# Kernel tuning notes

Hardware: AMD Instinct MI355X
Metric: run time of the kernel (lower is better)

Reference implementation:

```python
import jax, jax.numpy as jnp
import numpy as np

N_CLASSES = 5  # number of label classes in gts (mode is taken over these)


def setup_inputs() -> dict:
    key = jax.random.key(0)
    k1, k2, k3 = jax.random.split(key, 3)
    B, C, H, W = 4, 128, 512, 512
    n_tokens = 800      # superpixels per image (same for every image)
    max_length = 1024   # fixed sequence length -> pad = 224 per image
    features = jax.random.normal(k1, (B, C, H, W), dtype=jnp.float32)
    gts = jax.random.randint(k2, (B, H, W), 0, N_CLASSES, dtype=jnp.int32)
    segments = jax.random.randint(k3, (B, H, W), 0, n_tokens, dtype=jnp.int32)
    return {"features": features, "gts": gts, "segments": segments,
            "n_tokens": n_tokens, "max_length": max_length}


def reference(features, gts, segments, n_tokens, max_length):
    # Faithful vectorized form of IRGS_Trans.Extract_tokens with
    # mix_images=False, random_tokens=False:
    #   for each superpixel: token = mean of features over its pixels,
    #   label = mode of gts over its pixels; pack per-image into
    #   max_length sequences with zero padding; pads = max_length - n_tokens.
    B, C, H, W = features.shape
    num_seg = B * n_tokens

    # global segment ids (equivalent to the `segments[i] += s + 1` offsetting)
    seg = (segments + jnp.arange(B, dtype=segments.dtype)[:, None, None] * n_tokens).reshape(-1)

    # per-superpixel mean of features: [B*H*W, C] gathered into [B*n_tokens, C]
    feats = jnp.transpose(features, (0, 2, 3, 1)).reshape(-1, C)
    sums = jax.ops.segment_sum(feats, seg, num_segments=num_seg)
    cnt = jax.ops.segment_sum(jnp.ones((seg.shape[0],), feats.dtype), seg,
                              num_segments=num_seg)
    means = sums / jnp.maximum(cnt, 1.0)[:, None]

    # per-superpixel mode of gts via class histogram + argmax
    # (argmax returns the first/smallest class on ties, matching torch.mode)
    onehot = jax.nn.one_hot(gts.reshape(-1), N_CLASSES, dtype=jnp.float32)
    hist = jax.ops.segment_sum(onehot, seg, num_segments=num_seg)
    modes = jnp.argmax(hist, axis=-1).astype(jnp.float32)

    pad = max_length - n_tokens
    tokens = jnp.pad(means.reshape(B, n_tokens, C), ((0, 0), (0, pad), (0, 0)))
    super_labels = jnp.pad(modes.reshape(B, n_tokens), ((0, 0), (0, pad)))
    pads = jnp.full((B, 1), float(pad), dtype=jnp.float32)
    return tokens, super_labels, pads
```

## Files before the change

### kernel.cpp

```cpp
#include <hip/hip_runtime.h>

#define B_    4
#define C_    128
#define H_    512
#define W_    512
#define HW    (H_*W_)
#define NTOK  800
#define MAXLEN 1024
#define NCLS  5
#define NSEG  (B_*NTOK)

#define SCALE      262144.0f
#define INV_SCALE  (1.0f/262144.0f)

#define CG     8
#define NGRP   (C_/CG)
#define CHUNKS 32
#define CHUNK  (HW/CHUNKS)

#define HCHUNKS 64
#define HCHUNK  (HW/HCHUNKS)

#define HBINS   (NTOK*NCLS)
#define SEGBINS (CG*NTOK)

template <bool PARTIAL>
__global__ __launch_bounds__(256) void hist_kernel(const int* __restrict__ seg,
                                                   const int* __restrict__ gts,
                                                   int* __restrict__ hist) {
    __shared__ __align__(16) int lh[HBINS];
    for (int i = threadIdx.x; i < HBINS; i += 256) lh[i] = 0;
    __syncthreads();

    const int chunk = blockIdx.x, b = blockIdx.y;
    const int base = b * HW + chunk * HCHUNK;
    for (int tile = 0; tile < HCHUNK; tile += 1024) {
        const int idx = base + tile + threadIdx.x * 4;
        const int4 s4 = *(const int4*)(seg + idx);
        const int4 g4 = *(const int4*)(gts + idx);
        atomicAdd(&lh[s4.x * NCLS + g4.x], 1);
        atomicAdd(&lh[s4.y * NCLS + g4.y], 1);
        atomicAdd(&lh[s4.z * NCLS + g4.z], 1);
        atomicAdd(&lh[s4.w * NCLS + g4.w], 1);
    }
    __syncthreads();

    if (PARTIAL) {
        int* dst = hist + (size_t)(b * HCHUNKS + chunk) * HBINS;
        for (int i = threadIdx.x; i < HBINS / 4; i += 256)
            ((int4*)dst)[i] = ((const int4*)lh)[i];
    } else {
        int* gh = hist + b * HBINS;
        for (int i = threadIdx.x; i < HBINS; i += 256)
            atomicAdd(&gh[i], lh[i]);
    }
}

template <int NCH>
__global__ __launch_bounds__(256) void finalize_meta_kernel(const int* __restrict__ hist,
                                                            float* __restrict__ invs,
                                                            float* __restrict__ out) {
    const int tid = blockIdx.x * 256 + threadIdx.x;
    const int b = tid >> 10, t = tid & (MAXLEN - 1);
    float label = 0.0f;
    if (t < NTOK) {
        int h[NCLS] = {0, 0, 0, 0, 0};
        const int* hp = hist + (size_t)b * NCH * HBINS + t * NCLS;
#pragma unroll 4
        for (int ch = 0; ch < NCH; ++ch) {
#pragma unroll
            for (int k = 0; k < NCLS; ++k) h[k] += hp[(size_t)ch * HBINS + k];
        }
        int cnt = 0, best = -1, mode = 0;
#pragma unroll
        for (int k = 0; k < NCLS; ++k) {
            cnt += h[k];
            if (h[k] > best) { best = h[k]; mode = k; }
        }
        label = (float)mode;
        invs[b * NTOK + t] = INV_SCALE / (float)max(cnt, 1);
    }
    out[(size_t)B_ * MAXLEN * C_ + tid] = label;
    if (tid < B_) out[(size_t)B_ * MAXLEN * C_ + (size_t)B_ * MAXLEN + tid] =
        (float)(MAXLEN - NTOK);
}

template <bool PARTIAL>
__global__ __launch_bounds__(256, 6) void seg_sum_kernel(const float* __restrict__ feat,
                                                         const int* __restrict__ seg,
                                                         int* __restrict__ sums) {
    __shared__ __align__(16) int lsum[SEGBINS];
    for (int i = threadIdx.x; i < SEGBINS; i += 256) lsum[i] = 0;
    __syncthreads();

    const int chunk = blockIdx.x, grp = blockIdx.y, b = blockIdx.z;
    const int*   segp = seg  + (size_t)b * HW + chunk * CHUNK;
    const float* fp   = feat + ((size_t)b * C_ + (size_t)grp * CG) * HW + chunk * CHUNK;

    for (int tile = 0; tile < CHUNK; tile += 1024) {
        const int idx = tile + threadIdx.x * 4;
        const int4 s4 = *(const int4*)(segp + idx);
        float4 f[CG];
#pragma unroll
        for (int c = 0; c < CG; ++c)
            f[c] = *(const float4*)(fp + (size_t)c * HW + idx);
#pragma unroll
        for (int c = 0; c < CG; ++c) {
            atomicAdd(&lsum[c * NTOK + s4.x], __float2int_rn(f[c].x * SCALE));
            atomicAdd(&lsum[c * NTOK + s4.y], __float2int_rn(f[c].y * SCALE));
            atomicAdd(&lsum[c * NTOK + s4.z], __float2int_rn(f[c].z * SCALE));
            atomicAdd(&lsum[c * NTOK + s4.w], __float2int_rn(f[c].w * SCALE));
        }
    }
    __syncthreads();

    if (PARTIAL) {
        int* dst = sums + (size_t)((b * NGRP + grp) * CHUNKS + chunk) * SEGBINS;
        for (int i = threadIdx.x; i < SEGBINS / 4; i += 256)
            ((int4*)dst)[i] = ((const int4*)lsum)[i];
    } else {
        for (int i = threadIdx.x; i < SEGBINS; i += 256) {
            const int c = i / NTOK, s = i - c * NTOK;
            atomicAdd(&sums[((size_t)(b * NTOK + s)) * C_ + grp * CG + c], lsum[i]);
        }
    }
}

__global__ __launch_bounds__(1024) void reduce_sums_kernel(const int* __restrict__ part,
                                                           int* __restrict__ sums) {
    const int grp = blockIdx.x, b = blockIdx.y;
    const int* p = part + (size_t)(b * NGRP + grp) * CHUNKS * SEGBINS;
    for (int i = threadIdx.x; i < SEGBINS; i += 1024) {
        int acc = 0;
#pragma unroll 8
        for (int ch = 0; ch < CHUNKS; ++ch) acc += p[(size_t)ch * SEGBINS + i];
        const int c = i / NTOK, s = i - c * NTOK;
        sums[((size_t)(b * NTOK + s)) * C_ + grp * CG + c] = acc;
    }
}

__global__ __launch_bounds__(256) void tokens_kernel(const int* __restrict__ sums,
                                                     const float* __restrict__ invs,
                                                     float4* __restrict__ out4) {
    const int i = blockIdx.x * 256 + threadIdx.x;
    const int q = i & 31;
    const int tl = i >> 5;
    const int b = tl >> 10, t = tl & (MAXLEN - 1);
    float4 v = make_float4(0.f, 0.f, 0.f, 0.f);
    if (t < NTOK) {
        const int g = b * NTOK + t;
        const float s = invs[g];
        const int4 u = ((const int4*)sums)[(size_t)g * (C_ / 4) + q];
        v = make_float4((float)u.x * s, (float)u.y * s, (float)u.z * s, (float)u.w * s);
    }
    out4[i] = v;
}

extern "C" void kernel_launch(void* const* d_in, const int* in_sizes, int n_in,
                              void* d_out, int out_size, void* d_ws, size_t ws_size,
                              hipStream_t stream) {
    const float* feat = (const float*)d_in[0];
    const int*   gts  = (const int*)d_in[1];
    const int*   seg  = (const int*)d_in[2];
    float* out = (float*)d_out;

    char* ws = (char*)d_ws;
    const size_t sums_bytes  = (size_t)NSEG * C_ * sizeof(int);
    const size_t invs_bytes  = (size_t)NSEG * sizeof(float);
    const size_t histp_bytes = (size_t)B_ * HCHUNKS * HBINS * sizeof(int);
    const size_t segp_bytes  = (size_t)B_ * NGRP * CHUNKS * SEGBINS * sizeof(int);
    const size_t need_partial = sums_bytes + invs_bytes + histp_bytes + segp_bytes;

    if (ws_size >= need_partial) {
        int*   sums  = (int*)ws;
        float* invs  = (float*)(ws + sums_bytes);
        int*   histp = (int*)(ws + sums_bytes + invs_bytes);
        int*   segp  = (int*)(ws + sums_bytes + invs_bytes + histp_bytes);

        hist_kernel<true><<<dim3(HCHUNKS, B_), 256, 0, stream>>>(seg, gts, histp);
        finalize_meta_kernel<HCHUNKS><<<dim3((B_ * MAXLEN) / 256), 256, 0, stream>>>(
            histp, invs, out);
        seg_sum_kernel<true><<<dim3(CHUNKS, NGRP, B_), 256, 0, stream>>>(feat, seg, segp);
        reduce_sums_kernel<<<dim3(NGRP, B_), 1024, 0, stream>>>(segp, sums);
        tokens_kernel<<<dim3((B_ * MAXLEN * (C_ / 4)) / 256), 256, 0, stream>>>(
            sums, invs, (float4*)out);
    } else {
        const size_t hist_bytes = (size_t)NSEG * NCLS * sizeof(int);
        int*   sums = (int*)ws;
        int*   hist = (int*)(ws + sums_bytes);
        float* invs = (float*)(ws + sums_bytes + hist_bytes);

        hipMemsetAsync(ws, 0, sums_bytes + hist_bytes, stream);
        hist_kernel<false><<<dim3(HCHUNKS, B_), 256, 0, stream>>>(seg, gts, hist);
        finalize_meta_kernel<1><<<dim3((B_ * MAXLEN) / 256), 256, 0, stream>>>(
            hist, invs, out);
        seg_sum_kernel<false><<<dim3(CHUNKS, NGRP, B_), 256, 0, stream>>>(feat, seg, sums);
        tokens_kernel<<<dim3((B_ * MAXLEN * (C_ / 4)) / 256), 256, 0, stream>>>(
            sums, invs, (float4*)out);
    }
}
```

Before: 740.3 us.

## Pack two biased fixed-point channels into 64-bit LDS atomics for segment sums

Each pair of channels is biased to non-negative fixed-point values and packed into one 64-bit word, so each pixel issues half as many LDS atomic adds. Partial sums are stored as 64-bit words. The reduce kernel subtracts count*bias per lane using per-segment counts now saved by the finalize kernel. The risk is carry from the low 32-bit lane into the high lane if the biased partial sums overflow 32 bits, which depends on the feature magnitude and the number of pixels per bin.

```diff
diff --git a/kernel.cpp b/kernel.cpp
--- a/kernel.cpp
+++ b/kernel.cpp
@@ -13,7 +13,11 @@
 #define SCALE      262144.0f
 #define INV_SCALE  (1.0f/262144.0f)
 
+#define BIAS_F  2097152.0f
+#define BIAS_U  2097152u
+
 #define CG     8
+#define CPAIR  (CG/2)
 #define NGRP   (C_/CG)
 #define CHUNKS 32
 #define CHUNK  (HW/CHUNKS)
@@ -23,6 +27,7 @@
 
 #define HBINS   (NTOK*NCLS)
 #define SEGBINS (CG*NTOK)
+#define NBIN64  (CPAIR*NTOK)
 
 template <bool PARTIAL>
 __global__ __launch_bounds__(256) void hist_kernel(const int* __restrict__ seg,
@@ -59,6 +64,7 @@
 template <int NCH>
 __global__ __launch_bounds__(256) void finalize_meta_kernel(const int* __restrict__ hist,
                                                             float* __restrict__ invs,
+                                                            int* __restrict__ cnts,
                                                             float* __restrict__ out) {
     const int tid = blockIdx.x * 256 + threadIdx.x;
     const int b = tid >> 10, t = tid & (MAXLEN - 1);
@@ -79,14 +85,54 @@
         }
         label = (float)mode;
         invs[b * NTOK + t] = INV_SCALE / (float)max(cnt, 1);
+        cnts[b * NTOK + t] = cnt;
     }
     out[(size_t)B_ * MAXLEN * C_ + tid] = label;
     if (tid < B_) out[(size_t)B_ * MAXLEN * C_ + (size_t)B_ * MAXLEN + tid] =
         (float)(MAXLEN - NTOK);
 }
 
-template <bool PARTIAL>
-__global__ __launch_bounds__(256, 6) void seg_sum_kernel(const float* __restrict__ feat,
+__device__ __forceinline__ unsigned long long pack2(float x, float y) {
+    const unsigned lo = (unsigned)__float2int_rn(fmaf(x, SCALE, BIAS_F));
+    const unsigned hi = (unsigned)__float2int_rn(fmaf(y, SCALE, BIAS_F));
+    return ((unsigned long long)hi << 32) | lo;
+}
+
+__global__ __launch_bounds__(256, 6) void seg_sum_part(const float* __restrict__ feat,
+                                                       const int* __restrict__ seg,
+                                                       unsigned long long* __restrict__ part) {
+    __shared__ __align__(16) unsigned long long lsum[NBIN64];
+    for (int i = threadIdx.x; i < NBIN64; i += 256) lsum[i] = 0ull;
+    __syncthreads();
+
+    const int chunk = blockIdx.x, grp = blockIdx.y, b = blockIdx.z;
+    const int*   segp = seg  + (size_t)b * HW + chunk * CHUNK;
+    const float* fp   = feat + ((size_t)b * C_ + (size_t)grp * CG) * HW + chunk * CHUNK;
+
+    for (int tile = 0; tile < CHUNK; tile += 1024) {
+        const int idx = tile + threadIdx.x * 4;
+        const int4 s4 = *(const int4*)(segp + idx);
+        float4 f[CG];
+#pragma unroll
+        for (int c = 0; c < CG; ++c)
+            f[c] = *(const float4*)(fp + (size_t)c * HW + idx);
+#pragma unroll
+        for (int p = 0; p < CPAIR; ++p) {
+            const float4 a = f[2 * p], c = f[2 * p + 1];
+            atomicAdd(&lsum[p * NTOK + s4.x], pack2(a.x, c.x));
+            atomicAdd(&lsum[p * NTOK + s4.y], pack2(a.y, c.y));
+            atomicAdd(&lsum[p * NTOK + s4.z], pack2(a.z, c.z));
+            atomicAdd(&lsum[p * NTOK + s4.w], pack2(a.w, c.w));
+        }
+    }
+    __syncthreads();
+
+    unsigned long long* dst = part + (size_t)((b * NGRP + grp) * CHUNKS + chunk) * NBIN64;
+    for (int i = threadIdx.x; i < NBIN64 / 2; i += 256)
+        ((ulonglong2*)dst)[i] = ((const ulonglong2*)lsum)[i];
+}
+
+__global__ __launch_bounds__(256, 6) void seg_sum_atomic(const float* __restrict__ feat,
                                                          const int* __restrict__ seg,
                                                          int* __restrict__ sums) {
     __shared__ __align__(16) int lsum[SEGBINS];
@@ -114,28 +160,27 @@
     }
     __syncthreads();
 
-    if (PARTIAL) {
-        int* dst = sums + (size_t)((b * NGRP + grp) * CHUNKS + chunk) * SEGBINS;
-        for (int i = threadIdx.x; i < SEGBINS / 4; i += 256)
-            ((int4*)dst)[i] = ((const int4*)lsum)[i];
-    } else {
-        for (int i = threadIdx.x; i < SEGBINS; i += 256) {
-            const int c = i / NTOK, s = i - c * NTOK;
-            atomicAdd(&sums[((size_t)(b * NTOK + s)) * C_ + grp * CG + c], lsum[i]);
-        }
-    }
-}
-
-__global__ __launch_bounds__(1024) void reduce_sums_kernel(const int* __restrict__ part,
+    for (int i = threadIdx.x; i < SEGBINS; i += 256) {
+        const int c = i / NTOK, s = i - c * NTOK;
+        atomicAdd(&sums[((size_t)(b * NTOK + s)) * C_ + grp * CG + c], lsum[i]);
+    }
+}
+
+__global__ __launch_bounds__(1024) void reduce_sums_kernel(const unsigned long long* __restrict__ part,
+                                                           const int* __restrict__ cnts,
                                                            int* __restrict__ sums) {
     const int grp = blockIdx.x, b = blockIdx.y;
-    const int* p = part + (size_t)(b * NGRP + grp) * CHUNKS * SEGBINS;
-    for (int i = threadIdx.x; i < SEGBINS; i += 1024) {
-        int acc = 0;
+    const unsigned long long* p = part + (size_t)(b * NGRP + grp) * CHUNKS * NBIN64;
+    for (int i = threadIdx.x; i < NBIN64; i += 1024) {
+        unsigned long long acc = 0ull;
 #pragma unroll 8
-        for (int ch = 0; ch < CHUNKS; ++ch) acc += p[(size_t)ch * SEGBINS + i];
-        const int c = i / NTOK, s = i - c * NTOK;
-        sums[((size_t)(b * NTOK + s)) * C_ + grp * CG + c] = acc;
+        for (int ch = 0; ch < CHUNKS; ++ch) acc += p[(size_t)ch * NBIN64 + i];
+        const int pr = i / NTOK, s = i - pr * NTOK;
+        const unsigned corr = (unsigned)cnts[b * NTOK + s] * BIAS_U;
+        int2 v;
+        v.x = (int)((unsigned)acc - corr);
+        v.y = (int)((unsigned)(acc >> 32) - corr);
+        *(int2*)&sums[((size_t)(b * NTOK + s)) * C_ + grp * CG + 2 * pr] = v;
     }
 }
 
@@ -167,21 +212,24 @@
     char* ws = (char*)d_ws;
     const size_t sums_bytes  = (size_t)NSEG * C_ * sizeof(int);
     const size_t invs_bytes  = (size_t)NSEG * sizeof(float);
+    const size_t cnts_bytes  = (size_t)NSEG * sizeof(int);
     const size_t histp_bytes = (size_t)B_ * HCHUNKS * HBINS * sizeof(int);
-    const size_t segp_bytes  = (size_t)B_ * NGRP * CHUNKS * SEGBINS * sizeof(int);
-    const size_t need_partial = sums_bytes + invs_bytes + histp_bytes + segp_bytes;
+    const size_t segp_bytes  = (size_t)B_ * NGRP * CHUNKS * NBIN64 * 8;
+    const size_t need_partial = sums_bytes + invs_bytes + cnts_bytes + histp_bytes + segp_bytes;
 
     if (ws_size >= need_partial) {
         int*   sums  = (int*)ws;
         float* invs  = (float*)(ws + sums_bytes);
-        int*   histp = (int*)(ws + sums_bytes + invs_bytes);
-        int*   segp  = (int*)(ws + sums_bytes + invs_bytes + histp_bytes);
+        int*   cnts  = (int*)(ws + sums_bytes + invs_bytes);
+        int*   histp = (int*)(ws + sums_bytes + invs_bytes + cnts_bytes);
+        unsigned long long* segp =
+            (unsigned long long*)(ws + sums_bytes + invs_bytes + cnts_bytes + histp_bytes);
 
         hist_kernel<true><<<dim3(HCHUNKS, B_), 256, 0, stream>>>(seg, gts, histp);
         finalize_meta_kernel<HCHUNKS><<<dim3((B_ * MAXLEN) / 256), 256, 0, stream>>>(
-            histp, invs, out);
-        seg_sum_kernel<true><<<dim3(CHUNKS, NGRP, B_), 256, 0, stream>>>(feat, seg, segp);
-        reduce_sums_kernel<<<dim3(NGRP, B_), 1024, 0, stream>>>(segp, sums);
+            histp, invs, cnts, out);
+        seg_sum_part<<<dim3(CHUNKS, NGRP, B_), 256, 0, stream>>>(feat, seg, segp);
+        reduce_sums_kernel<<<dim3(NGRP, B_), 1024, 0, stream>>>(segp, cnts, sums);
         tokens_kernel<<<dim3((B_ * MAXLEN * (C_ / 4)) / 256), 256, 0, stream>>>(
             sums, invs, (float4*)out);
     } else {
@@ -189,12 +237,13 @@
         int*   sums = (int*)ws;
         int*   hist = (int*)(ws + sums_bytes);
         float* invs = (float*)(ws + sums_bytes + hist_bytes);
+        int*   cnts = (int*)(ws + sums_bytes + hist_bytes + invs_bytes);
 
         hipMemsetAsync(ws, 0, sums_bytes + hist_bytes, stream);
         hist_kernel<false><<<dim3(HCHUNKS, B_), 256, 0, stream>>>(seg, gts, hist);
         finalize_meta_kernel<1><<<dim3((B_ * MAXLEN) / 256), 256, 0, stream>>>(
-            hist, invs, out);
-        seg_sum_kernel<false><<<dim3(CHUNKS, NGRP, B_), 256, 0, stream>>>(feat, seg, sums);
+            hist, invs, cnts, out);
+        seg_sum_atomic<<<dim3(CHUNKS, NGRP, B_), 256, 0, stream>>>(feat, seg, sums);
         tokens_kernel<<<dim3((B_ * MAXLEN * (C_ / 4)) / 256), 256, 0, stream>>>(
             sums, invs, (float4*)out);
     }
```

Result: no change. 739.5 us (-0.1%).
